# Kernel optimization log

Measured on AMD Instinct MI355X. Metric: run time of the kernel, lower is better.

The kernel has to match this reference:

```python
import jax, jax.numpy as jnp
import numpy as np

EPS = 1e-7


def _make_boxes(key, b, n):
    k1, k2 = jax.random.split(key)
    xy = jax.random.uniform(k1, (b, n, 2), dtype=jnp.float32)
    wh = jax.random.uniform(k2, (b, n, 2), dtype=jnp.float32) * 0.2 + 0.01
    return jnp.concatenate([xy, xy + wh], axis=-1)  # [B,N,4] xyxy, valid boxes


def setup_inputs() -> dict:
    key = jax.random.key(0)
    kp, kt = jax.random.split(key)
    B, P, T = 64, 2048, 256
    return {
        "pred_bboxes": _make_boxes(kp, B, P),
        "target_bboxes": _make_boxes(kt, B, T),
    }


def _pairwise_cost(pred, target):
    # pred: [B,P,4], target: [B,T,4] -> cost [T,P] = mean_b (1 - IoU)
    p = pred[:, None, :, :]    # [B,1,P,4]
    t = target[:, :, None, :]  # [B,T,1,4]
    ix1 = jnp.maximum(p[..., 0], t[..., 0])
    iy1 = jnp.maximum(p[..., 1], t[..., 1])
    ix2 = jnp.minimum(p[..., 2], t[..., 2])
    iy2 = jnp.minimum(p[..., 3], t[..., 3])
    inter = jnp.clip(ix2 - ix1, 0.0) * jnp.clip(iy2 - iy1, 0.0)  # [B,T,P]
    area_p = (p[..., 2] - p[..., 0]) * (p[..., 3] - p[..., 1])
    area_t = (t[..., 2] - t[..., 0]) * (t[..., 3] - t[..., 1])
    union = area_p + area_t - inter
    iou = inter / (union + EPS)
    return jnp.mean(1.0 - iou, axis=0)  # [T,P]


def _greedy_match_loss(cost):
    # Sequential greedy: for each target (in order) pick the still-available
    # pred with minimal loss, remove it, accumulate. Matches the torch loop
    # (ties -> lowest index; 1-IoU losses are always >= 0).
    T, P = cost.shape

    def step(mask, cost_row):
        masked = jnp.where(mask, cost_row, jnp.inf)
        k = jnp.argmin(masked)
        loss = masked[k]
        return mask.at[k].set(False), loss

    _, losses = jax.lax.scan(step, jnp.ones((P,), dtype=bool), cost)
    return jnp.sum(losses) / T


def reference(pred_bboxes, target_bboxes):
    cost = _pairwise_cost(pred_bboxes, target_bboxes)  # [T,P]
    return _greedy_match_loss(cost)
```

## Files before the change

kernel.cpp:

```cpp
#include <hip/hip_runtime.h>
#include <hip/hip_bf16.h>

typedef unsigned long long u64;
typedef unsigned int u32;

#define NB 64
#define NP 2048
#define NT 256
#define TK 8
#define RB 8
#define TT 8
#define PB 64
#define EPSF 1e-7f

__device__ inline float iou1(const float4 pb, const float ap,
                             const float4 tb, const float at_eps) {
    float ix1 = fmaxf(pb.x, tb.x);
    float iy1 = fmaxf(pb.y, tb.y);
    float ix2 = fminf(pb.z, tb.z);
    float iy2 = fminf(pb.w, tb.w);
    float dx = fmaxf(ix2 - ix1, 0.f);
    float dy = fmaxf(iy2 - iy1, 0.f);
    float inter = dx * dy;
    float uni = (ap + at_eps) - inter;
    return inter * __builtin_amdgcn_rcpf(uni);
}

__global__ __launch_bounds__(512) void cost_kernel(const float4* __restrict__ pred,
                                                   const float* __restrict__ tgt,
                                                   float* __restrict__ cost) {
    __shared__ float4 sT[NB * TT];
    __shared__ __align__(16) float sAf[NB * TT];
    __shared__ float sRed[8][TT][PB];
    const int tid = threadIdx.x;
    const int wv = tid >> 6, lane = tid & 63;
    const int p = blockIdx.x * PB + lane;
    const int t0 = blockIdx.y * TT;

    {
        int b = tid >> 3, tt = tid & 7;
        float4 tb = *(const float4*)&tgt[(b * NT + t0 + tt) * 4];
        sT[tid] = tb;
        sAf[tid] = (tb.z - tb.x) * (tb.w - tb.y) + EPSF;
    }
    __syncthreads();

    float acc[TT] = {0.f, 0.f, 0.f, 0.f, 0.f, 0.f, 0.f, 0.f};

    const int b0 = wv * (NB / 8);
    {
        float4 pb[8];
#pragma unroll
        for (int u = 0; u < 8; ++u) pb[u] = pred[(b0 + u) * NP + p];
#pragma unroll
        for (int u = 0; u < 8; ++u) {
            const int b = b0 + u;
            const float ap = (pb[u].z - pb[u].x) * (pb[u].w - pb[u].y);
#pragma unroll
            for (int tt = 0; tt < TT; ++tt) {
                acc[tt] += iou1(pb[u], ap, sT[b * TT + tt], sAf[b * TT + tt]);
            }
        }
    }
#pragma unroll
    for (int tt = 0; tt < TT; ++tt) sRed[wv][tt][lane] = acc[tt];
    __syncthreads();

    {
        const int tt = tid >> 6, l = tid & 63;
        float s = 0.f;
#pragma unroll
        for (int w = 0; w < 8; ++w) s += sRed[w][tt][l];
        cost[(size_t)(t0 + tt) * NP + blockIdx.x * PB + l] = 1.f - s * (1.f / NB);
    }
}

__device__ inline u64 wave_min_u64(u64 k) {
#pragma unroll
    for (int off = 1; off < 64; off <<= 1) {
        u32 lo = (u32)__shfl_xor((int)(u32)k, off);
        u32 hi = (u32)__shfl_xor((int)(u32)(k >> 32), off);
        u64 o = ((u64)hi << 32) | lo;
        if (o < k) k = o;
    }
    return k;
}

__global__ __launch_bounds__(256) void topk_kernel(const float* __restrict__ cost,
                                                   u64* __restrict__ toplist) {
    __shared__ u64 sK[32];
    const int tid = threadIdx.x;
    const int wv = tid >> 6, lane = tid & 63;
    const int t = blockIdx.x;
    const float* row = cost + (size_t)t * NP;

    float v[8];
#pragma unroll
    for (int c = 0; c < 2; ++c) {
        float4 q = *(const float4*)(row + wv * 512 + c * 256 + 4 * lane);
        v[4 * c + 0] = q.x; v[4 * c + 1] = q.y;
        v[4 * c + 2] = q.z; v[4 * c + 3] = q.w;
    }
    u32 used = 0;
    for (int e = 0; e < TK; ++e) {
        u64 best = ~0ull;
        u32 bs = 0;
#pragma unroll
        for (int s = 0; s < 8; ++s) {
            u32 hb = ((used >> s) & 1u) ? 0xFFFFFFFFu : __float_as_uint(v[s]);
            u32 gidx = (u32)(wv * 512 + (s >> 2) * 256 + 4 * lane + (s & 3));
            u64 key = ((u64)hb << 32) | gidx;
            if (key < best) { best = key; bs = (u32)s; }
        }
        u64 g = wave_min_u64(best);
        if (best == g) used |= (1u << bs);
        if (lane == 0) sK[wv * TK + e] = g;
    }
    __syncthreads();
    if (wv == 0) {
        u64 k = (lane < 32) ? sK[lane] : ~0ull;
        for (int e = 0; e < TK; ++e) {
            u64 g = wave_min_u64(k);
            if (k == g) k = ~0ull;
            if (lane == 0) toplist[t * TK + e] = g;
        }
    }
}

__device__ void fallback_pick(const float* __restrict__ row, u32 m, int lane,
                              u32* pickIdx, float* pickVal) {
    u64 best = ~0ull;
#pragma unroll 1
    for (int k = 0; k < 8; ++k) {
        float4 q = *(const float4*)(row + k * 256 + 4 * lane);
        float vv[4] = {q.x, q.y, q.z, q.w};
#pragma unroll
        for (int e = 0; e < 4; ++e) {
            u32 gidx = (u32)(k * 256 + 4 * lane + e);
            int w = __builtin_amdgcn_ds_bpermute((int)((gidx >> 5) << 2), (int)m);
            bool taken = (((u32)w >> (gidx & 31)) & 1u) != 0u;
            u32 hb = taken ? 0xFFFFFFFFu : __float_as_uint(vv[e]);
            u64 key = ((u64)hb << 32) | gidx;
            if (key < best) best = key;
        }
    }
    best = wave_min_u64(best);
    *pickIdx = (u32)best & (NP - 1);
    *pickVal = __uint_as_float((u32)(best >> 32));
}

__global__ __launch_bounds__(64) void greedy_kernel(const u64* __restrict__ toplist,
                                                    const float* __restrict__ cost,
                                                    float* __restrict__ out) {
    const int lane = threadIdx.x;
    u32 idxr[32], vbr[32];
#pragma unroll
    for (int k = 0; k < 32; ++k) {
        u64 v = toplist[64 * k + lane];
        idxr[k] = (u32)v & (NP - 1);
        vbr[k] = (u32)(v >> 32);
    }

    u32 m = 0;
    float sum = 0.f;
    u64 A = ~0ull;

#pragma unroll
    for (int k = 0; k < 32; ++k) {
        const u32 idx = idxr[k];
        const u32 vb = vbr[k];
        int wn = 0;
        if (k < 31)
            wn = __builtin_amdgcn_ds_bpermute((int)((idxr[k + 1] >> 5) << 2), (int)m);

        u32 pk[RB];
#pragma unroll
        for (int gg = 0; gg < RB; ++gg) {
            u64 bal = A & (0xFFull << (8 * gg));
            u32 pickIdx; float pickVal;
            if (bal != 0) {
                int f = (int)__ffsll(bal) - 1;
                pickIdx = (u32)__builtin_amdgcn_readlane((int)idx, f);
                pickVal = __uint_as_float((u32)__builtin_amdgcn_readlane((int)vb, f));
            } else {
                fallback_pick(cost + (size_t)(k * RB + gg) * NP, m, lane,
                              &pickIdx, &pickVal);
            }
            pk[gg] = pickIdx;
            sum += pickVal;
            if ((pickIdx >> 5) == (u32)lane) m |= (1u << (pickIdx & 31));
            A &= ~__ballot(idx == pickIdx);
        }

        if (k < 31) {
            const u32 idn = idxr[k + 1];
            u64 An = __ballot((((u32)wn >> (idn & 31)) & 1u) == 0u);
#pragma unroll
            for (int gg = 0; gg < RB; ++gg)
                An &= ~__ballot(idn == pk[gg]);
            A = An;
        }
    }
    if (lane == 0) out[0] = sum * (1.f / NT);
}

extern "C" void kernel_launch(void* const* d_in, const int* in_sizes, int n_in,
                              void* d_out, int out_size, void* d_ws, size_t ws_size,
                              hipStream_t stream) {
    const float4* pred = (const float4*)d_in[0];
    const float* tgt = (const float*)d_in[1];
    char* ws = (char*)d_ws;
    float* cost  = (float*)ws;
    u64* toplist = (u64*)(ws + (size_t)NT * NP * 4);

    cost_kernel<<<dim3(NP / PB, NT / TT), 512, 0, stream>>>(pred, tgt, cost);
    topk_kernel<<<NT, 256, 0, stream>>>(cost, toplist);
    greedy_kernel<<<1, 64, 0, stream>>>(toplist, cost, (float*)d_out);
}
```

Before: 52.40 us.

## Process two pred columns per thread in cost kernel with vectorized reduction

Each thread in the cost kernel now handles two prediction boxes (PB raised to 128), so every target box read from shared memory is reused for two IoU evaluations. Target areas are recomputed in registers rather than stored in a separate shared array. The final reduction runs on half the threads and uses float4 loads and stores to write the cost matrix. The grid is halved, which lowers parallelism, and register pressure rises; the launch bounds now request 4 blocks per CU.

Result: no change. 52.42 us (+0.0%).

```diff
diff --git a/kernel.cpp b/kernel.cpp
--- a/kernel.cpp
+++ b/kernel.cpp
@@ -10,7 +10,7 @@
 #define TK 8
 #define RB 8
 #define TT 8
-#define PB 64
+#define PB 128
 #define EPSF 1e-7f
 
 __device__ inline float iou1(const float4 pb, const float ap,
@@ -26,52 +26,62 @@
     return inter * __builtin_amdgcn_rcpf(uni);
 }
 
-__global__ __launch_bounds__(512) void cost_kernel(const float4* __restrict__ pred,
-                                                   const float* __restrict__ tgt,
-                                                   float* __restrict__ cost) {
+__global__ __launch_bounds__(512, 4) void cost_kernel(const float4* __restrict__ pred,
+                                                      const float* __restrict__ tgt,
+                                                      float* __restrict__ cost) {
     __shared__ float4 sT[NB * TT];
-    __shared__ __align__(16) float sAf[NB * TT];
     __shared__ float sRed[8][TT][PB];
     const int tid = threadIdx.x;
     const int wv = tid >> 6, lane = tid & 63;
-    const int p = blockIdx.x * PB + lane;
+    const int p0 = blockIdx.x * PB + lane;
     const int t0 = blockIdx.y * TT;
 
     {
         int b = tid >> 3, tt = tid & 7;
-        float4 tb = *(const float4*)&tgt[(b * NT + t0 + tt) * 4];
-        sT[tid] = tb;
-        sAf[tid] = (tb.z - tb.x) * (tb.w - tb.y) + EPSF;
+        sT[tid] = *(const float4*)&tgt[(b * NT + t0 + tt) * 4];
     }
     __syncthreads();
 
-    float acc[TT] = {0.f, 0.f, 0.f, 0.f, 0.f, 0.f, 0.f, 0.f};
-
-    const int b0 = wv * (NB / 8);
-    {
-        float4 pb[8];
-#pragma unroll
-        for (int u = 0; u < 8; ++u) pb[u] = pred[(b0 + u) * NP + p];
-#pragma unroll
-        for (int u = 0; u < 8; ++u) {
-            const int b = b0 + u;
-            const float ap = (pb[u].z - pb[u].x) * (pb[u].w - pb[u].y);
-#pragma unroll
-            for (int tt = 0; tt < TT; ++tt) {
-                acc[tt] += iou1(pb[u], ap, sT[b * TT + tt], sAf[b * TT + tt]);
-            }
-        }
-    }
-#pragma unroll
-    for (int tt = 0; tt < TT; ++tt) sRed[wv][tt][lane] = acc[tt];
+    float acc0[TT] = {0.f, 0.f, 0.f, 0.f, 0.f, 0.f, 0.f, 0.f};
+    float acc1[TT] = {0.f, 0.f, 0.f, 0.f, 0.f, 0.f, 0.f, 0.f};
+
+    const int b0 = wv * 8;
+#pragma unroll
+    for (int i = 0; i < 8; ++i) {
+        const int b = b0 + i;
+        const float4 pa = pred[b * NP + p0];
+        const float4 pc = pred[b * NP + p0 + 64];
+        const float apa = (pa.z - pa.x) * (pa.w - pa.y);
+        const float apc = (pc.z - pc.x) * (pc.w - pc.y);
+#pragma unroll
+        for (int tt = 0; tt < TT; ++tt) {
+            const float4 tb = sT[b * TT + tt];
+            const float at = (tb.z - tb.x) * (tb.w - tb.y) + EPSF;
+            acc0[tt] += iou1(pa, apa, tb, at);
+            acc1[tt] += iou1(pc, apc, tb, at);
+        }
+    }
+#pragma unroll
+    for (int tt = 0; tt < TT; ++tt) {
+        sRed[wv][tt][lane] = acc0[tt];
+        sRed[wv][tt][lane + 64] = acc1[tt];
+    }
     __syncthreads();
 
-    {
-        const int tt = tid >> 6, l = tid & 63;
-        float s = 0.f;
-#pragma unroll
-        for (int w = 0; w < 8; ++w) s += sRed[w][tt][l];
-        cost[(size_t)(t0 + tt) * NP + blockIdx.x * PB + l] = 1.f - s * (1.f / NB);
+    if (tid < 256) {
+        const int tt = tid >> 5, q = tid & 31;
+        float4 s = {0.f, 0.f, 0.f, 0.f};
+#pragma unroll
+        for (int w = 0; w < 8; ++w) {
+            float4 a = *(const float4*)&sRed[w][tt][q * 4];
+            s.x += a.x; s.y += a.y; s.z += a.z; s.w += a.w;
+        }
+        float4 c;
+        c.x = 1.f - s.x * (1.f / NB);
+        c.y = 1.f - s.y * (1.f / NB);
+        c.z = 1.f - s.z * (1.f / NB);
+        c.w = 1.f - s.w * (1.f / NB);
+        *(float4*)&cost[(size_t)(t0 + tt) * NP + blockIdx.x * PB + q * 4] = c;
     }
 }
 
```
